# Optimization experiments

Hardware: AMD Instinct MI355X
Metric: run time of the kernel (lower is better)

The kernel has to match this reference:

```python
import jax, jax.numpy as jnp
import numpy as np

B, CIN, H, W = 8, 3, 128, 128
D_MODEL = 256
N_LAYERS = 4
D_STATE = 16
D_CONV = 4
EXPAND = 2
HEADDIM = 64
D_INNER = EXPAND * D_MODEL            # 512
NHEADS = D_INNER // HEADDIM           # 8
CONV_DIM = D_INNER + 2 * D_STATE      # 544
D_IN_PROJ = 2 * D_INNER + 2 * D_STATE + NHEADS  # 1064
D_OUT = 10
EPS = 1e-5


def setup_inputs() -> dict:
    key = jax.random.key(0)
    ks = iter(jax.random.split(key, 64))
    nrm = lambda shape, s=0.02: jax.random.normal(next(ks), shape, jnp.float32) * s
    L = N_LAYERS
    # dt init in [1e-3, 0.1], dt_bias = inverse softplus of dt
    dt = jnp.exp(jax.random.uniform(next(ks), (L, NHEADS)) * (np.log(0.1) - np.log(1e-3)) + np.log(1e-3))
    dt_bias = dt + jnp.log(-jnp.expm1(-dt))
    A_log = jnp.log(jax.random.uniform(next(ks), (L, NHEADS), minval=1.0, maxval=16.0))
    return {
        "x": jax.random.normal(next(ks), (B, CIN, H, W), jnp.float32),
        "stem_w1": nrm((D_MODEL // 2, CIN, 3, 3), 0.1),
        "stem_g1": jnp.ones((D_MODEL // 2,), jnp.float32),
        "stem_b1": jnp.zeros((D_MODEL // 2,), jnp.float32),
        "stem_w2": nrm((D_MODEL, D_MODEL // 2, 4, 4), 0.05),
        "stem_g2": jnp.ones((D_MODEL,), jnp.float32),
        "stem_b2": jnp.zeros((D_MODEL,), jnp.float32),
        "in_w": nrm((L, D_MODEL, D_IN_PROJ)),
        "conv_w": nrm((L, CONV_DIM, D_CONV), 0.2),
        "conv_b": jnp.zeros((L, CONV_DIM), jnp.float32),
        "dt_bias": dt_bias,
        "A_log": A_log,
        "D_skip": jnp.ones((L, NHEADS), jnp.float32),
        "rms_w": jnp.ones((L, D_INNER), jnp.float32),
        "out_w": nrm((L, D_INNER, D_MODEL)),
        "ln_g": jnp.ones((L, D_MODEL), jnp.float32),
        "ln_b": jnp.zeros((L, D_MODEL), jnp.float32),
        "head_ln_g": jnp.ones((D_MODEL,), jnp.float32),
        "head_ln_b": jnp.zeros((D_MODEL,), jnp.float32),
        "head_w": nrm((D_MODEL, D_OUT)),
        "head_b": jnp.zeros((D_OUT,), jnp.float32),
    }


def _bn(x, g, b):  # eval-mode BatchNorm2d with running mean 0 / var 1
    return x * g[None, :, None, None] + b[None, :, None, None]


def _ln(x, g, b):
    m = jnp.mean(x, -1, keepdims=True)
    v = jnp.mean((x - m) ** 2, -1, keepdims=True)
    return (x - m) * jax.lax.rsqrt(v + EPS) * g + b


def _mamba2(x, in_w, conv_w, conv_b, dt_bias, A_log, D_skip, rms_w, out_w):
    Bb, Lq, _ = x.shape
    zxbcdt = x @ in_w                                        # (B,L,D_IN_PROJ)
    z = zxbcdt[..., :D_INNER]
    xBC = zxbcdt[..., D_INNER:D_INNER + CONV_DIM]
    dt = jax.nn.softplus(zxbcdt[..., -NHEADS:] + dt_bias)    # (B,L,H)
    # causal depthwise conv1d over time
    xp = jnp.pad(xBC, ((0, 0), (D_CONV - 1, 0), (0, 0)))
    xBC = sum(xp[:, k:k + Lq, :] * conv_w[:, k] for k in range(D_CONV)) + conv_b
    xBC = jax.nn.silu(xBC)
    xs = xBC[..., :D_INNER].reshape(Bb, Lq, NHEADS, HEADDIM)       # (B,L,H,P)
    Bm = xBC[..., D_INNER:D_INNER + D_STATE]                        # (B,L,N)
    Cm = xBC[..., D_INNER + D_STATE:]                               # (B,L,N)
    dA = jnp.exp(dt * (-jnp.exp(A_log)))                            # (B,L,H)
    dtx = xs * dt[..., None]                                        # (B,L,H,P)

    def step(h, inp):  # h: (B,H,P,N)
        dA_t, dtx_t, B_t, C_t = inp
        h = h * dA_t[:, :, None, None] + dtx_t[..., None] * B_t[:, None, None, :]
        y = jnp.einsum('bhpn,bn->bhp', h, C_t)
        return h, y

    h0 = jnp.zeros((Bb, NHEADS, HEADDIM, D_STATE), x.dtype)
    seq = (jnp.moveaxis(dA, 1, 0), jnp.moveaxis(dtx, 1, 0),
           jnp.moveaxis(Bm, 1, 0), jnp.moveaxis(Cm, 1, 0))
    _, ys = jax.lax.scan(step, h0, seq)                             # (L,B,H,P)
    y = jnp.moveaxis(ys, 0, 1) + xs * D_skip[None, None, :, None]
    y = y.reshape(Bb, Lq, D_INNER)
    y = y * jax.nn.silu(z)                                          # gated
    y = y * jax.lax.rsqrt(jnp.mean(y * y, -1, keepdims=True) + EPS) * rms_w
    return y @ out_w


def reference(x, stem_w1, stem_g1, stem_b1, stem_w2, stem_g2, stem_b2,
              in_w, conv_w, conv_b, dt_bias, A_log, D_skip, rms_w, out_w,
              ln_g, ln_b, head_ln_g, head_ln_b, head_w, head_b):
    dn = ('NCHW', 'OIHW', 'NCHW')
    h = jax.lax.conv_general_dilated(x, stem_w1, (1, 1), 'SAME', dimension_numbers=dn)
    h = jax.nn.gelu(_bn(h, stem_g1, stem_b1), approximate=False)
    h = jax.lax.conv_general_dilated(h, stem_w2, (4, 4), 'VALID', dimension_numbers=dn)
    h = jax.nn.gelu(_bn(h, stem_g2, stem_b2), approximate=False)
    tok = h.reshape(h.shape[0], D_MODEL, -1).transpose(0, 2, 1)     # (B,L,D)
    for i in range(N_LAYERS):
        m = _mamba2(tok, in_w[i], conv_w[i], conv_b[i], dt_bias[i],
                    A_log[i], D_skip[i], rms_w[i], out_w[i])
        tok = _ln(m + tok, ln_g[i], ln_b[i])
    pooled = tok.mean(1)
    return _ln(pooled, head_ln_g, head_ln_b) @ head_w + head_b
```

## Files before the change

kernel.cpp:

```cpp
#include <hip/hip_runtime.h>
#include <hip/hip_bf16.h>


#define DEV __device__ __forceinline__
typedef __hip_bfloat16 bf16;
typedef unsigned short ushort_t;
typedef __attribute__((ext_vector_type(8))) short s8v;
typedef __attribute__((ext_vector_type(8))) unsigned short u8v;
typedef __attribute__((ext_vector_type(4))) unsigned short u4v;
typedef __attribute__((ext_vector_type(4))) float f4v;

#define CHUNK 32
#define NCH 32

#define SP_CONVW 0
#define SP_CONVB 8704
#define SP_DTB   10880
#define SP_ALOG  10912
#define SP_DSK   10944
#define SP_RMSW  10976
#define SP_LNG   13024
#define SP_LNB   14048
#define SP_HLG   15072
#define SP_HLB   15328
#define SP_HW    15584
#define SP_HB    18144
#define SP_G1    18160
#define SP_B1    18288
#define SP_G2    18416
#define SP_B2    18672
#define SP_TOTAL 18928

DEV float bf2f(bf16 h) { return __bfloat162float(h); }
DEV bf16 f2bf(float f) { return __float2bfloat16(f); }
DEV float us2f(ushort_t u) { return __uint_as_float(((unsigned int)u) << 16); }
DEV ushort_t f2bfs(float f) {
    unsigned int u = __float_as_uint(f);
    return (ushort_t)((u + 0x7FFFu + ((u >> 16) & 1u)) >> 16);
}
DEV float ldf(const void* p, size_t i, int bf) {
    return bf ? us2f(((const ushort_t*)p)[i]) : ((const float*)p)[i];
}
DEV ushort_t ldbf(const void* p, size_t i, int bf) {
    return bf ? ((const ushort_t*)p)[i] : f2bfs(((const float*)p)[i]);
}
DEV int mode_of(const void* g1) { return (((const unsigned int*)g1)[0] == 0x3F800000u) ? 0 : 1; }
DEV float sigmoidf_(float x) { return 1.f / (1.f + __expf(-x)); }
DEV float geluf_(float x) { return 0.5f * x * (1.f + erff(x * 0.70710678118654752f)); }

__global__ void k_prep(const void* cw, const void* cb, const void* dtb, const void* alog,
                       const void* dsk, const void* rmsw, const void* lng, const void* lnb,
                       const void* hlg, const void* hlb, const void* hw, const void* hb,
                       const void* g1, const void* b1, const void* g2, const void* b2,
                       const void* w1, const void* w2, const void* inw, const void* outw,
                       float* __restrict__ sp, ushort_t* __restrict__ wT) {
    int md = mode_of(g1);
    int i = blockIdx.x * 256 + threadIdx.x;
    if (i < SP_TOTAL) {
        float v;
        if (i < SP_CONVB) v = ldf(cw, i, md);
        else if (i < SP_DTB) v = ldf(cb, i - SP_CONVB, md);
        else if (i < SP_ALOG) v = ldf(dtb, i - SP_DTB, md);
        else if (i < SP_DSK) v = ldf(alog, i - SP_ALOG, md);
        else if (i < SP_RMSW) v = ldf(dsk, i - SP_DSK, md);
        else if (i < SP_LNG) v = ldf(rmsw, i - SP_RMSW, md);
        else if (i < SP_LNB) v = ldf(lng, i - SP_LNG, md);
        else if (i < SP_HLG) v = ldf(lnb, i - SP_LNB, md);
        else if (i < SP_HLB) v = ldf(hlg, i - SP_HLG, md);
        else if (i < SP_HW) v = ldf(hlb, i - SP_HLB, md);
        else if (i < SP_HB) v = ldf(hw, i - SP_HW, md);
        else if (i < SP_G1) v = (i - SP_HB < 10) ? ldf(hb, i - SP_HB, md) : 0.f;
        else if (i < SP_B1) v = ldf(g1, i - SP_G1, md);
        else if (i < SP_G2) v = ldf(b1, i - SP_B1, md);
        else if (i < SP_B2) v = ldf(g2, i - SP_G2, md);
        else v = ldf(b2, i - SP_B2, md);
        sp[i] = v;
        return;
    }
    int iw = i - SP_TOTAL;
    if (iw >= 2142208) return;
    ushort_t v;
    if (iw < 4096) {
        int oc = iw >> 5, k = iw & 31;
        v = (k < 27) ? ldbf(w1, (size_t)oc * 27 + k, md) : 0;
    } else if (iw < 528384) {
        int j = iw - 4096;
        int oc = j >> 11, k = j & 2047;
        int c = k & 127, kykx = k >> 7;
        v = ldbf(w2, (size_t)(oc * 128 + c) * 16 + kykx, md);
    } else if (iw < 1617920) {
        int j = iw - 528384;
        int l = j / 272384, r = j % 272384;
        int n = r >> 8, k = r & 255;
        v = ldbf(inw, (size_t)l * 272384 + (size_t)k * 1064 + n, md);
    } else {
        int j = iw - 1617920;
        int l = j >> 17, r = j & 131071;
        int n = r >> 9, k = r & 511;
        v = ldbf(outw, (size_t)l * 131072 + (size_t)k * 256 + n, md);
    }
    wT[iw] = v;
}

template <int MD>
DEV void im2col_body(const void* x, ushort_t* __restrict__ Aim, int m) {
    int xx = m & 127;
    int y = (m >> 7) & 127;
    int b = m >> 14;
    ushort_t* o = Aim + (size_t)m * 32;
#pragma unroll
    for (int ci = 0; ci < 3; ci++)
#pragma unroll
        for (int dy = 0; dy < 3; dy++) {
            int sy = y + dy - 1;
#pragma unroll
            for (int dx = 0; dx < 3; dx++) {
                int sx = xx + dx - 1;
                ushort_t v = 0;
                if (sy >= 0 && sy < 128 && sx >= 0 && sx < 128) {
                    size_t idx = (size_t)((b * 3 + ci) * 128 + sy) * 128 + sx;
                    v = MD ? ((const ushort_t*)x)[idx] : f2bfs(((const float*)x)[idx]);
                }
                o[ci * 9 + dy * 3 + dx] = v;
            }
        }
#pragma unroll
    for (int k = 27; k < 32; k++) o[k] = 0;
}
__global__ void k_im2col(const void* __restrict__ x, ushort_t* __restrict__ Aim,
                         const void* __restrict__ g1) {
    int m = blockIdx.x * 256 + threadIdx.x;
    if (m >= 131072) return;
    if (mode_of(g1)) im2col_body<1>(x, Aim, m);
    else im2col_body<0>(x, Aim, m);
}

template <int EPI, int CBF, int BK>
__global__ __launch_bounds__(256, 3) void k_gemmT(const ushort_t* __restrict__ A,
                                                  const ushort_t* __restrict__ Wt, void* __restrict__ C,
                                                  int M, int N, int K, int klen,
                                                  const float* __restrict__ g, const float* __restrict__ bb) {
    constexpr int KG = BK / 8;
    constexpr int EA = BK / 4;
    constexpr int EB = BK / 2;
    constexpr int AU = EA / 8;
    constexpr int BU = EB / 8;
    __shared__ __align__(16) ushort_t As[2][64 * BK];
    __shared__ __align__(16) ushort_t Bs[2][128 * BK];
    int tid = threadIdx.x;
    int m0 = blockIdx.y * 64, n0 = blockIdx.x * 128;
    int koff = blockIdx.z * klen;
    int w = tid >> 6, lane = tid & 63;
    int wm = (w >> 1) * 32, wn = (w & 1) * 64;
    int lm = lane & 15, quad = lane >> 4;
    int ar = tid >> 2, ak = (tid & 3) * EA;
    int br = tid >> 1, bk = (tid & 1) * EB;
    bool bvalid = (n0 + br) < N;

    u8v pa[AU], pb[BU];
    auto loadT = [&](int kb) {
        const u8v* ap = (const u8v*)(A + (size_t)(m0 + ar) * K + koff + kb + ak);
#pragma unroll
        for (int j = 0; j < AU; j++) pa[j] = ap[j];
        if (bvalid) {
            const u8v* bp = (const u8v*)(Wt + (size_t)(n0 + br) * K + koff + kb + bk);
#pragma unroll
            for (int j = 0; j < BU; j++) pb[j] = bp[j];
        } else {
#pragma unroll
            for (int j = 0; j < BU; j++) pb[j] = (u8v)0;
        }
    };
    auto storeT = [&](int buf) {
        int ag = ak >> 3;
#pragma unroll
        for (int j = 0; j < AU; j++)
            *(u8v*)&As[buf][((ar >> 4) * KG + ag + j) * 128 + (ar & 15) * 8] = pa[j];
        int bg = bk >> 3;
#pragma unroll
        for (int j = 0; j < BU; j++)
            *(u8v*)&Bs[buf][((br >> 4) * KG + bg + j) * 128 + (br & 15) * 8] = pb[j];
    };

    f4v acc[2][4];
#pragma unroll
    for (int i = 0; i < 2; i++)
#pragma unroll
        for (int j = 0; j < 4; j++) acc[i][j] = (f4v){0.f, 0.f, 0.f, 0.f};

    int niter = klen / BK;
    loadT(0);
    storeT(0);
    if (niter > 1) loadT(BK);
    __syncthreads();
    for (int it = 0; it < niter; it++) {
        int buf = it & 1;
        if (it + 1 < niter) {
            storeT(buf ^ 1);
            if (it + 2 < niter) loadT((it + 2) * BK);
        }
#pragma unroll
        for (int kk = 0; kk < BK / 32; kk++) {
            s8v af[2], bfr[4];
#pragma unroll
            for (int i = 0; i < 2; i++)
                af[i] = *(const s8v*)&As[buf][(((wm >> 4) + i) * KG + kk * 4 + quad) * 128 + lm * 8];
#pragma unroll
            for (int j = 0; j < 4; j++)
                bfr[j] = *(const s8v*)&Bs[buf][(((wn >> 4) + j) * KG + kk * 4 + quad) * 128 + lm * 8];
#pragma unroll
            for (int i = 0; i < 2; i++)
#pragma unroll
                for (int j = 0; j < 4; j++)
                    acc[i][j] = __builtin_amdgcn_mfma_f32_16x16x32_bf16(af[i], bfr[j], acc[i][j], 0, 0, 0);
        }
        __syncthreads();
    }
    float* Cz = (float*)C + (size_t)blockIdx.z * M * N;
#pragma unroll
    for (int i = 0; i < 2; i++)
#pragma unroll
        for (int j = 0; j < 4; j++) {
            int nn = n0 + wn + j * 16 + lm;
            if (nn >= N) continue;
            float gv = (EPI >= 1) ? g[nn] : 0.f, bv = (EPI >= 1) ? bb[nn] : 0.f;
#pragma unroll
            for (int rr = 0; rr < 4; rr++) {
                int mm = m0 + wm + i * 16 + quad * 4 + rr;
                float v = acc[i][j][rr];
                if (EPI >= 1) v = geluf_(v * gv + bv);
                if (EPI == 2) {
                    int b = mm >> 14, y = (mm >> 7) & 127, x = mm & 127;
                    size_t mp = (size_t)(b * 1024 + (y >> 2) * 32 + (x >> 2));
                    ((bf16*)C)[mp * 2048 + ((y & 3) * 4 + (x & 3)) * 128 + nn] = f2bf(v);
                } else if (CBF) {
                    ((bf16*)C)[(size_t)mm * N + nn] = f2bf(v);
                } else {
                    Cz[(size_t)mm * N + nn] = v;
                }
            }
        }
}

__global__ __launch_bounds__(256) void k_stemred(const float* __restrict__ parts, const float* __restrict__ sp,
                                                 float* __restrict__ tok, ushort_t* __restrict__ tokb) {
    int m = blockIdx.x, c = threadIdx.x;
    size_t off = (size_t)m * 256 + c;
    float s = parts[off] + parts[2097152 + off];
    float v = geluf_(s * sp[SP_G2 + c] + sp[SP_B2 + c]);
    tok[off] = v;
    tokb[off] = f2bfs(v);
}

__global__ __launch_bounds__(64) void k_scan1(const bf16* __restrict__ zx, const float* __restrict__ sp,
                                              float* __restrict__ Sbuf, float* __restrict__ Pbuf, int layer) {
    int bid = blockIdx.x;
    int c = bid & (NCH - 1);
    int bh = bid >> 5;
    int b = bh >> 3, h = bh & 7;
    int p = threadIdx.x;
    __shared__ __align__(16) ushort_t zraw[35 * 64];
    __shared__ __align__(16) ushort_t braw[35 * 32];
    __shared__ float xs_s[CHUNK * 64];
    __shared__ __align__(16) float bc_s[CHUNK * 32];
    __shared__ float da_s[CHUNK], dt_s[CHUNK];
    const ushort_t* zxB = (const ushort_t*)zx + (size_t)b * 1024 * 1064;
    int t0 = c * CHUNK;
#pragma unroll
    for (int k = 0; k < 5; k++) {
        int j = p + k * 64;
        if (j < 280) {
            int row = j >> 3, c8 = j & 7;
            int t = t0 - 3 + row;
            u8v v = (u8v)0;
            if (t >= 0) v = *(const u8v*)(zxB + (size_t)t * 1064 + 512 + h * 64 + c8 * 8);
            *(u8v*)&zraw[row * 64 + c8 * 8] = v;
        }
    }
#pragma unroll
    for (int k = 0; k < 3; k++) {
        int j = p + k * 64;
        if (j < 140) {
            int row = j >> 2, c8 = j & 3;
            int t = t0 - 3 + row;
            u8v v = (u8v)0;
            if (t >= 0) v = *(const u8v*)(zxB + (size_t)t * 1064 + 1024 + c8 * 8);
            *(u8v*)&braw[row * 32 + c8 * 8] = v;
        }
    }
    if (p < CHUNK) {
        float raw = bf2f(zx[(size_t)(b * 1024 + t0 + p) * 1064 + 1056 + h]) + sp[SP_DTB + layer * 8 + h];
        float dt = raw > 20.f ? raw : log1pf(expf(raw));
        float a = expf(sp[SP_ALOG + layer * 8 + h]);
        dt_s[p] = dt;
        da_s[p] = expf(-dt * a);
    }
    __syncthreads();
    {
        const float* wp = sp + SP_CONVW + (size_t)(layer * 544 + h * 64 + p) * 4;
        float w0 = wp[0], w1 = wp[1], w2 = wp[2], w3 = wp[3];
        float bias = sp[SP_CONVB + layer * 544 + h * 64 + p];
#pragma unroll 8
        for (int tt = 0; tt < CHUNK; tt++) {
            float acc = bias + us2f(zraw[tt * 64 + p]) * w0 + us2f(zraw[(tt + 1) * 64 + p]) * w1 +
                        us2f(zraw[(tt + 2) * 64 + p]) * w2 + us2f(zraw[(tt + 3) * 64 + p]) * w3;
            xs_s[tt * 64 + p] = acc * sigmoidf_(acc);
        }
    }
    if (p < 32) {
        const float* wp = sp + SP_CONVW + (size_t)(layer * 544 + 512 + p) * 4;
        float w0 = wp[0], w1 = wp[1], w2 = wp[2], w3 = wp[3];
        float bias = sp[SP_CONVB + layer * 544 + 512 + p];
        int n = p & 15;
        int slot = (p < 16) ? 2 * n : 2 * n + 1;
#pragma unroll 8
        for (int tt = 0; tt < CHUNK; tt++) {
            float acc = bias + us2f(braw[tt * 32 + p]) * w0 + us2f(braw[(tt + 1) * 32 + p]) * w1 +
                        us2f(braw[(tt + 2) * 32 + p]) * w2 + us2f(braw[(tt + 3) * 32 + p]) * w3;
            bc_s[tt * 32 + slot] = acc * sigmoidf_(acc);
        }
    }
    __syncthreads();
    float hs[16];
#pragma unroll
    for (int n = 0; n < 16; n++) hs[n] = 0.f;
    float P = 1.f;
    for (int tt = 0; tt < CHUNK; tt++) {
        float xsv = xs_s[tt * 64 + p];
        float dAv = da_s[tt], dtv = dt_s[tt];
        P *= dAv;
        float dtx = xsv * dtv;
        const float4* bcp = (const float4*)&bc_s[tt * 32];
#pragma unroll
        for (int j = 0; j < 8; j++) {
            float4 v = bcp[j];
            hs[2 * j] = hs[2 * j] * dAv + dtx * v.x;
            hs[2 * j + 1] = hs[2 * j + 1] * dAv + dtx * v.z;
        }
    }
    float* So = Sbuf + (size_t)bid * 1024;
#pragma unroll
    for (int n = 0; n < 16; n++) So[n * 64 + p] = hs[n];
    if (p == 0) Pbuf[bid] = P;
}

__global__ __launch_bounds__(256) void k_scan2(const float* __restrict__ Sbuf, const float* __restrict__ Pbuf,
                                               float* __restrict__ Hbuf) {
    int bh = blockIdx.x >> 2;
    int e = ((blockIdx.x & 3) << 8) + threadIdx.x;
    const float* Sp = Sbuf + (size_t)bh * NCH * 1024 + e;
    float* Hp = Hbuf + (size_t)bh * NCH * 1024 + e;
    float hh = 0.f;
#pragma unroll
    for (int gq = 0; gq < 4; gq++) {
        float s[8];
#pragma unroll
        for (int c2 = 0; c2 < 8; c2++) s[c2] = Sp[(size_t)(gq * 8 + c2) * 1024];
#pragma unroll
        for (int c2 = 0; c2 < 8; c2++) {
            Hp[(size_t)(gq * 8 + c2) * 1024] = hh;
            float P = Pbuf[bh * NCH + gq * 8 + c2];
            hh = P * hh + s[c2];
        }
    }
}

__global__ __launch_bounds__(512, 2) void k_scan3g(const bf16* __restrict__ zx,
                                                   const float* __restrict__ Hbuf,
                                                   const float* __restrict__ sp, bf16* __restrict__ y,
                                                   int layer) {
    int bid = blockIdx.x;
    int c = bid & 31;
    int b = bid >> 5;
    int tid = threadIdx.x;
    int h = tid >> 6, p = tid & 63;
    __shared__ __align__(16) ushort_t zraw[35 * 512];
    __shared__ __align__(16) ushort_t braw[35 * 32];
    __shared__ __align__(16) float bc_s[CHUNK * 32];
    __shared__ float da_s[8 * CHUNK], dt_s[8 * CHUNK];
    const ushort_t* zxB = (const ushort_t*)zx + (size_t)b * 1024 * 1064;
    int t0 = c * CHUNK;

#pragma unroll
    for (int k = 0; k < 5; k++) {
        int j = tid + k * 512;
        if (j < 2240) {
            int row = j >> 6, c8 = j & 63;
            int t = t0 - 3 + row;
            u8v v = (u8v)0;
            if (t >= 0) v = *(const u8v*)(zxB + (size_t)t * 1064 + 512 + c8 * 8);
            *(u8v*)&zraw[row * 512 + c8 * 8] = v;
        }
    }
    if (tid < 140) {
        int row = tid >> 2, c8 = tid & 3;
        int t = t0 - 3 + row;
        u8v v = (u8v)0;
        if (t >= 0) v = *(const u8v*)(zxB + (size_t)t * 1064 + 1024 + c8 * 8);
        *(u8v*)&braw[row * 32 + c8 * 8] = v;
    }
    if (tid < 256) {
        int tt = tid >> 3, hh = tid & 7;
        float raw = bf2f(zx[(size_t)(b * 1024 + t0 + tt) * 1064 + 1056 + hh]) + sp[SP_DTB + layer * 8 + hh];
        float dtv = raw > 20.f ? raw : log1pf(expf(raw));
        float a = expf(sp[SP_ALOG + layer * 8 + hh]);
        dt_s[hh * 32 + tt] = dtv;
        da_s[hh * 32 + tt] = expf(-dtv * a);
    }
    __syncthreads();

    float xs[CHUNK];
    {
        float4 w4 = *(const float4*)(sp + SP_CONVW + (size_t)(layer * 544 + tid) * 4);
        float bias = sp[SP_CONVB + layer * 544 + tid];
#pragma unroll
        for (int tt = 0; tt < CHUNK; tt++) {
            float acc = bias + us2f(zraw[tt * 512 + tid]) * w4.x + us2f(zraw[(tt + 1) * 512 + tid]) * w4.y +
                        us2f(zraw[(tt + 2) * 512 + tid]) * w4.z + us2f(zraw[(tt + 3) * 512 + tid]) * w4.w;
            xs[tt] = acc * sigmoidf_(acc);
        }
    }
    if (tid < 32) {
        float4 w4 = *(const float4*)(sp + SP_CONVW + (size_t)(layer * 544 + 512 + tid) * 4);
        float bias = sp[SP_CONVB + layer * 544 + 512 + tid];
        int n = tid & 15;
        int slot = (tid < 16) ? 2 * n : 2 * n + 1;
#pragma unroll
        for (int tt = 0; tt < CHUNK; tt++) {
            float acc = bias + us2f(braw[tt * 32 + tid]) * w4.x + us2f(braw[(tt + 1) * 32 + tid]) * w4.y +
                        us2f(braw[(tt + 2) * 32 + tid]) * w4.z + us2f(braw[(tt + 3) * 32 + tid]) * w4.w;
            bc_s[tt * 32 + slot] = acc * sigmoidf_(acc);
        }
    }

    float hs[16];
    {
        const float* Si = Hbuf + ((size_t)(b * 8 + h) * 32 + c) * 1024;
#pragma unroll
        for (int n = 0; n < 16; n++) hs[n] = Si[n * 64 + p];
    }
    float dsk = sp[SP_DSK + layer * 8 + h];
    __syncthreads();

    ushort_t* y_s = zraw;
#pragma unroll
    for (int tt = 0; tt < CHUNK; tt++) {
        float dAv = da_s[h * 32 + tt], dtv = dt_s[h * 32 + tt];
        float dtx = xs[tt] * dtv;
        float acc = 0.f;
        const float4* bcp = (const float4*)&bc_s[tt * 32];
#pragma unroll
        for (int j = 0; j < 8; j++) {
            float4 v = bcp[j];
            hs[2 * j] = hs[2 * j] * dAv + dtx * v.x;
            acc += hs[2 * j] * v.y;
            hs[2 * j + 1] = hs[2 * j + 1] * dAv + dtx * v.z;
            acc += hs[2 * j + 1] * v.w;
        }
        y_s[tt * 512 + tid] = f2bfs(acc + xs[tt] * dsk);
    }
    __syncthreads();

    {
        int lane = p;
        float4 rw0 = *(const float4*)(sp + SP_RMSW + layer * 512 + lane * 8);
        float4 rw1 = *(const float4*)(sp + SP_RMSW + layer * 512 + lane * 8 + 4);
        float rwv[8] = {rw0.x, rw0.y, rw0.z, rw0.w, rw1.x, rw1.y, rw1.z, rw1.w};
#pragma unroll
        for (int r = 0; r < 4; r++) {
            int tt = h * 4 + r;
            u8v yv = *(const u8v*)&y_s[tt * 512 + lane * 8];
            u8v zv = *(const u8v*)(zxB + (size_t)(t0 + tt) * 1064 + lane * 8);
            float t[8];
            float ss = 0.f;
#pragma unroll
            for (int j2 = 0; j2 < 8; j2++) {
                float z = us2f(zv[j2]);
                float yy = us2f(yv[j2]);
                float tv = yy * (z * sigmoidf_(z));
                t[j2] = tv;
                ss += tv * tv;
            }
#pragma unroll
            for (int d = 32; d; d >>= 1) ss += __shfl_xor(ss, d, 64);
            float scale = rsqrtf(ss * (1.f / 512.f) + 1e-5f);
            u8v o;
#pragma unroll
            for (int j2 = 0; j2 < 8; j2++) o[j2] = f2bfs(t[j2] * scale * rwv[j2]);
            *(u8v*)((ushort_t*)y + (size_t)(b * 1024 + t0 + tt) * 512 + lane * 8) = o;
        }
    }
}

DEV float block_sum256(float v, float* s4) {
#pragma unroll
    for (int off = 32; off; off >>= 1) v += __shfl_down(v, off, 64);
    __syncthreads();
    if ((threadIdx.x & 63) == 0) s4[threadIdx.x >> 6] = v;
    __syncthreads();
    return s4[0] + s4[1] + s4[2] + s4[3];
}

__global__ __launch_bounds__(256) void k_resln(float* __restrict__ tok, ushort_t* __restrict__ tokb,
                                               const float* __restrict__ parts, const float* __restrict__ sp,
                                               int layer) {
    int w = threadIdx.x >> 6, lane = threadIdx.x & 63;
    int m = blockIdx.x * 4 + w;
    size_t off = (size_t)m * 256 + lane * 4;
    float4 v = *(const float4*)(tok + off);
    float4 p0 = *(const float4*)(parts + off);
    float4 p1 = *(const float4*)(parts + 2097152 + off);
    v.x += p0.x + p1.x;
    v.y += p0.y + p1.y;
    v.z += p0.z + p1.z;
    v.w += p0.w + p1.w;
    float s = v.x + v.y + v.z + v.w;
#pragma unroll
    for (int d = 32; d; d >>= 1) s += __shfl_xor(s, d, 64);
    float mean = s * (1.f / 256.f);
    float dx = v.x - mean, dy = v.y - mean, dz = v.z - mean, dw = v.w - mean;
    float ss = dx * dx + dy * dy + dz * dz + dw * dw;
#pragma unroll
    for (int d = 32; d; d >>= 1) ss += __shfl_xor(ss, d, 64);
    float inv = rsqrtf(ss * (1.f / 256.f) + 1e-5f);
    const float* lg = sp + SP_LNG + layer * 256 + lane * 4;
    const float* lb = sp + SP_LNB + layer * 256 + lane * 4;
    float r0 = dx * inv * lg[0] + lb[0];
    float r1 = dy * inv * lg[1] + lb[1];
    float r2 = dz * inv * lg[2] + lb[2];
    float r3 = dw * inv * lg[3] + lb[3];
    float4 r;
    r.x = r0; r.y = r1; r.z = r2; r.w = r3;
    *(float4*)(tok + off) = r;
    u4v ob;
    ob[0] = f2bfs(r0); ob[1] = f2bfs(r1); ob[2] = f2bfs(r2); ob[3] = f2bfs(r3);
    *(u4v*)(tokb + off) = ob;
}

__global__ void k_pool1(const float* __restrict__ tok, float* __restrict__ ppart) {
    int b = blockIdx.x >> 4, chunk = blockIdx.x & 15;
    int c = threadIdx.x;
    float s = 0.f;
    for (int t = 0; t < 64; t++) s += tok[((size_t)b * 1024 + chunk * 64 + t) * 256 + c];
    ppart[(size_t)blockIdx.x * 256 + c] = s;
}

__global__ __launch_bounds__(256) void k_head(const float* __restrict__ ppart, const float* __restrict__ sp,
                                              void* __restrict__ out, const void* __restrict__ g1) {
    __shared__ float s4[4];
    __shared__ float lds[256];
    int md = mode_of(g1);
    int b = blockIdx.x;
    int c = threadIdx.x;
    float v = 0.f;
#pragma unroll
    for (int k = 0; k < 16; k++) v += ppart[(size_t)(b * 16 + k) * 256 + c];
    v *= (1.f / 1024.f);
    float mean = block_sum256(v, s4) * (1.f / 256.f);
    float d = v - mean;
    float var = block_sum256(d * d, s4) * (1.f / 256.f);
    lds[c] = d * rsqrtf(var + 1e-5f) * sp[SP_HLG + c] + sp[SP_HLB + c];
    __syncthreads();
    if (c < 10) {
        float s = sp[SP_HB + c];
        for (int k = 0; k < 256; k++) s += lds[k] * sp[SP_HW + k * 10 + c];
        if (md)
            ((bf16*)out)[b * 10 + c] = f2bf(s);
        else
            ((float*)out)[b * 10 + c] = s;
    }
}

extern "C" void kernel_launch(void* const* d_in, const int* in_sizes, int n_in, void* d_out, int out_size,
                              void* d_ws, size_t ws_size, hipStream_t stream) {
    const void* x         = d_in[0];
    const void* stem_w1   = d_in[1];
    const void* stem_g1   = d_in[2];
    const void* stem_b1   = d_in[3];
    const void* stem_w2   = d_in[4];
    const void* stem_g2   = d_in[5];
    const void* stem_b2   = d_in[6];
    const void* in_w      = d_in[7];
    const void* conv_w    = d_in[8];
    const void* conv_b    = d_in[9];
    const void* dt_bias   = d_in[10];
    const void* A_log     = d_in[11];
    const void* D_skip    = d_in[12];
    const void* rms_w     = d_in[13];
    const void* out_w     = d_in[14];
    const void* ln_g      = d_in[15];
    const void* ln_b      = d_in[16];
    const void* head_ln_g = d_in[17];
    const void* head_ln_b = d_in[18];
    const void* head_w    = d_in[19];
    const void* head_b    = d_in[20];

    float* ws     = (float*)d_ws;
    float* tok    = ws;
    float* mbuf   = ws + 2097152;
    float* Hbuf   = ws + 4194304;
    float* parts  = ws + 6291456;
    float* ppart  = ws + 14682112;
    float* Pbuf   = ws + 14714880;
    float* sp     = ws + 14716944;
    ushort_t* tokb = (ushort_t*)(ws + 14735888);
    ushort_t* wT  = (ushort_t*)(ws + 15784464);
    ushort_t* w1T   = wT;
    ushort_t* w2T   = wT + 4096;
    ushort_t* inwT  = wT + 528384;
    ushort_t* outwT = wT + 1617920;
    bf16* arena   = (bf16*)(ws + 16855568);
    bf16* zx      = arena;
    bf16* ybuf    = arena + 13172736;
    ushort_t* patch = (ushort_t*)arena;
    ushort_t* Aim  = (ushort_t*)mbuf;
    float* Sbuf    = mbuf;

    k_prep<<<(SP_TOTAL + 2142208 + 255) / 256, 256, 0, stream>>>(
        conv_w, conv_b, dt_bias, A_log, D_skip, rms_w, ln_g, ln_b, head_ln_g, head_ln_b, head_w, head_b,
        stem_g1, stem_b1, stem_g2, stem_b2, stem_w1, stem_w2, in_w, out_w, sp, wT);

    k_im2col<<<512, 256, 0, stream>>>(x, Aim, stem_g1);
    k_gemmT<2, 1, 32><<<dim3(1, 2048, 1), 256, 0, stream>>>(Aim, w1T, patch, 131072, 128, 32, 32,
                                                            sp + SP_G1, sp + SP_B1);
    k_gemmT<0, 0, 64><<<dim3(2, 128, 2), 256, 0, stream>>>(patch, w2T, parts, 8192, 256, 2048, 1024,
                                                           nullptr, nullptr);
    k_stemred<<<8192, 256, 0, stream>>>(parts, sp, tok, tokb);

    for (int l = 0; l < 4; l++) {
        k_gemmT<0, 1, 64><<<dim3(9, 128, 1), 256, 0, stream>>>(tokb, inwT + (size_t)l * 272384, zx, 8192,
                                                               1064, 256, 256, nullptr, nullptr);
        k_scan1<<<2048, 64, 0, stream>>>(zx, sp, Sbuf, Pbuf, l);
        k_scan2<<<256, 256, 0, stream>>>(Sbuf, Pbuf, Hbuf);
        k_scan3g<<<256, 512, 0, stream>>>(zx, Hbuf, sp, ybuf, l);
        k_gemmT<0, 0, 64><<<dim3(2, 128, 2), 256, 0, stream>>>((const ushort_t*)ybuf,
                                                               outwT + (size_t)l * 131072, parts, 8192, 256,
                                                               512, 256, nullptr, nullptr);
        k_resln<<<8192 / 4, 256, 0, stream>>>(tok, tokb, parts, sp, l);
    }

    k_pool1<<<128, 256, 0, stream>>>(tok, ppart);
    k_head<<<8, 256, 0, stream>>>(ppart, sp, d_out, stem_g1);
}
```

Measured before the change: 483.1 us.

## Add 128x128 double-buffered MFMA GEMM for stem and in-projection

Adds a new GEMM kernel with 128x128 output tiles, register-prefetched double-buffered shared memory, and each wave computing a 64x64 sub-tile with bf16 MFMA. The stem second conv and the per-layer in-projection use it, and the stem conv split-K goes from 2 to 4 partial slices, so the reduction kernel now sums four partial buffers. The aim is more reuse per loaded tile and fewer global loads. The cost is higher register and LDS use per block, a larger parts buffer, and extra reduction traffic. The out-projection GEMM is left on the old kernel.

```diff
diff --git a/kernel.cpp b/kernel.cpp
--- a/kernel.cpp
+++ b/kernel.cpp
@@ -242,11 +242,102 @@
         }
 }
 
+template <int CBF>
+__global__ __launch_bounds__(256, 2) void k_gemm128(const ushort_t* __restrict__ A,
+                                                    const ushort_t* __restrict__ Wt, void* __restrict__ C,
+                                                    int M, int N, int K, int klen) {
+    constexpr int BK = 64;
+    constexpr int KG = BK / 8;
+    __shared__ __align__(16) ushort_t As[2][128 * BK];
+    __shared__ __align__(16) ushort_t Bs[2][128 * BK];
+    int tid = threadIdx.x;
+    int m0 = blockIdx.y * 128, n0 = blockIdx.x * 128;
+    int koff = blockIdx.z * klen;
+    int w = tid >> 6, lane = tid & 63;
+    int wm = (w >> 1) * 64, wn = (w & 1) * 64;
+    int lm = lane & 15, quad = lane >> 4;
+    int r = tid >> 1, ck = (tid & 1) * 32;
+    bool bvalid = (n0 + r) < N;
+
+    u8v pa[4], pb[4];
+    auto loadT = [&](int kb) {
+        const u8v* ap = (const u8v*)(A + (size_t)(m0 + r) * K + koff + kb + ck);
+#pragma unroll
+        for (int j = 0; j < 4; j++) pa[j] = ap[j];
+        if (bvalid) {
+            const u8v* bp = (const u8v*)(Wt + (size_t)(n0 + r) * K + koff + kb + ck);
+#pragma unroll
+            for (int j = 0; j < 4; j++) pb[j] = bp[j];
+        } else {
+#pragma unroll
+            for (int j = 0; j < 4; j++) pb[j] = (u8v)0;
+        }
+    };
+    auto storeT = [&](int buf) {
+        int g = ck >> 3;
+#pragma unroll
+        for (int j = 0; j < 4; j++) {
+            *(u8v*)&As[buf][((r >> 4) * KG + g + j) * 128 + (r & 15) * 8] = pa[j];
+            *(u8v*)&Bs[buf][((r >> 4) * KG + g + j) * 128 + (r & 15) * 8] = pb[j];
+        }
+    };
+
+    f4v acc[4][4];
+#pragma unroll
+    for (int i = 0; i < 4; i++)
+#pragma unroll
+        for (int j = 0; j < 4; j++) acc[i][j] = (f4v){0.f, 0.f, 0.f, 0.f};
+
+    int niter = klen / BK;
+    loadT(0);
+    storeT(0);
+    if (niter > 1) loadT(BK);
+    __syncthreads();
+    for (int it = 0; it < niter; it++) {
+        int buf = it & 1;
+        if (it + 1 < niter) {
+            storeT(buf ^ 1);
+            if (it + 2 < niter) loadT((it + 2) * BK);
+        }
+#pragma unroll
+        for (int kk = 0; kk < 2; kk++) {
+            s8v af[4], bfr[4];
+#pragma unroll
+            for (int i = 0; i < 4; i++)
+                af[i] = *(const s8v*)&As[buf][(((wm >> 4) + i) * KG + kk * 4 + quad) * 128 + lm * 8];
+#pragma unroll
+            for (int j = 0; j < 4; j++)
+                bfr[j] = *(const s8v*)&Bs[buf][(((wn >> 4) + j) * KG + kk * 4 + quad) * 128 + lm * 8];
+#pragma unroll
+            for (int i = 0; i < 4; i++)
+#pragma unroll
+                for (int j = 0; j < 4; j++)
+                    acc[i][j] = __builtin_amdgcn_mfma_f32_16x16x32_bf16(af[i], bfr[j], acc[i][j], 0, 0, 0);
+        }
+        __syncthreads();
+    }
+    float* Cz = (float*)C + (size_t)blockIdx.z * M * N;
+#pragma unroll
+    for (int i = 0; i < 4; i++)
+#pragma unroll
+        for (int j = 0; j < 4; j++) {
+            int nn = n0 + wn + j * 16 + lm;
+            if (nn >= N) continue;
+#pragma unroll
+            for (int rr = 0; rr < 4; rr++) {
+                int mm = m0 + wm + i * 16 + quad * 4 + rr;
+                float v = acc[i][j][rr];
+                if (CBF) ((bf16*)C)[(size_t)mm * N + nn] = f2bf(v);
+                else Cz[(size_t)mm * N + nn] = v;
+            }
+        }
+}
+
 __global__ __launch_bounds__(256) void k_stemred(const float* __restrict__ parts, const float* __restrict__ sp,
                                                  float* __restrict__ tok, ushort_t* __restrict__ tokb) {
     int m = blockIdx.x, c = threadIdx.x;
     size_t off = (size_t)m * 256 + c;
-    float s = parts[off] + parts[2097152 + off];
+    float s = parts[off] + parts[2097152 + off] + parts[2 * 2097152 + off] + parts[3 * 2097152 + off];
     float v = geluf_(s * sp[SP_G2 + c] + sp[SP_B2 + c]);
     tok[off] = v;
     tokb[off] = f2bfs(v);
@@ -623,13 +714,12 @@
     k_im2col<<<512, 256, 0, stream>>>(x, Aim, stem_g1);
     k_gemmT<2, 1, 32><<<dim3(1, 2048, 1), 256, 0, stream>>>(Aim, w1T, patch, 131072, 128, 32, 32,
                                                             sp + SP_G1, sp + SP_B1);
-    k_gemmT<0, 0, 64><<<dim3(2, 128, 2), 256, 0, stream>>>(patch, w2T, parts, 8192, 256, 2048, 1024,
-                                                           nullptr, nullptr);
+    k_gemm128<0><<<dim3(2, 64, 4), 256, 0, stream>>>(patch, w2T, parts, 8192, 256, 2048, 512);
     k_stemred<<<8192, 256, 0, stream>>>(parts, sp, tok, tokb);
 
     for (int l = 0; l < 4; l++) {
-        k_gemmT<0, 1, 64><<<dim3(9, 128, 1), 256, 0, stream>>>(tokb, inwT + (size_t)l * 272384, zx, 8192,
-                                                               1064, 256, 256, nullptr, nullptr);
+        k_gemm128<1><<<dim3(9, 64, 1), 256, 0, stream>>>(tokb, inwT + (size_t)l * 272384, zx, 8192,
+                                                         1064, 256, 256);
         k_scan1<<<2048, 64, 0, stream>>>(zx, sp, Sbuf, Pbuf, l);
         k_scan2<<<256, 256, 0, stream>>>(Sbuf, Pbuf, Hbuf);
         k_scan3g<<<256, 512, 0, stream>>>(zx, Hbuf, sp, ybuf, l);
```

Result: no change. 491.6 us (+1.8%).

## Fuse out-projection GEMM and residual LayerNorm into the scan-output kernel

Applied to the files above, without the earlier changes.

The scan-output kernel now keeps its gated, RMS-normalised y chunk (32 tokens × 512) in padded LDS. It runs the out-projection there with bf16 MFMA, each of the 8 waves computing 32 output columns against weights read from global memory. It then adds the residual and applies LayerNorm in place, which removes the y buffer round trip, the split-K partial sums and two kernel launches per layer. The cost is that each block re-reads the full 256KB out-projection weight from global/L2 with only 256 blocks, and the LDS row stride is padded to avoid bank conflicts.

```diff
diff --git a/kernel.cpp b/kernel.cpp
--- a/kernel.cpp
+++ b/kernel.cpp
@@ -12,6 +12,7 @@
 
 #define CHUNK 32
 #define NCH 32
+#define YST 520
 
 #define SP_CONVW 0
 #define SP_CONVB 8704
@@ -365,10 +366,12 @@
     }
 }
 
-__global__ __launch_bounds__(512, 2) void k_scan3g(const bf16* __restrict__ zx,
-                                                   const float* __restrict__ Hbuf,
-                                                   const float* __restrict__ sp, bf16* __restrict__ y,
-                                                   int layer) {
+__global__ __launch_bounds__(512, 2) void k_scan3go(const bf16* __restrict__ zx,
+                                                    const float* __restrict__ Hbuf,
+                                                    const float* __restrict__ sp,
+                                                    const ushort_t* __restrict__ Wt,
+                                                    float* __restrict__ tok, ushort_t* __restrict__ tokb,
+                                                    int layer) {
     int bid = blockIdx.x;
     int c = bid & 31;
     int b = bid >> 5;
@@ -457,7 +460,7 @@
             hs[2 * j + 1] = hs[2 * j + 1] * dAv + dtx * v.z;
             acc += hs[2 * j + 1] * v.w;
         }
-        y_s[tt * 512 + tid] = f2bfs(acc + xs[tt] * dsk);
+        y_s[tt * YST + tid] = f2bfs(acc + xs[tt] * dsk);
     }
     __syncthreads();
 
@@ -469,7 +472,7 @@
 #pragma unroll
         for (int r = 0; r < 4; r++) {
             int tt = h * 4 + r;
-            u8v yv = *(const u8v*)&y_s[tt * 512 + lane * 8];
+            u8v yv = *(const u8v*)&y_s[tt * YST + lane * 8];
             u8v zv = *(const u8v*)(zxB + (size_t)(t0 + tt) * 1064 + lane * 8);
             float t[8];
             float ss = 0.f;
@@ -487,8 +490,75 @@
             u8v o;
 #pragma unroll
             for (int j2 = 0; j2 < 8; j2++) o[j2] = f2bfs(t[j2] * scale * rwv[j2]);
-            *(u8v*)((ushort_t*)y + (size_t)(b * 1024 + t0 + tt) * 512 + lane * 8) = o;
-        }
+            *(u8v*)&y_s[tt * YST + lane * 8] = o;
+        }
+    }
+    __syncthreads();
+
+    int lm = p & 15, quad = p >> 4;
+    f4v acc2[2][2];
+#pragma unroll
+    for (int mi = 0; mi < 2; mi++)
+#pragma unroll
+        for (int ni = 0; ni < 2; ni++) acc2[mi][ni] = (f4v){0.f, 0.f, 0.f, 0.f};
+#pragma unroll
+    for (int kk = 0; kk < 16; kk++) {
+        s8v af[2], bw[2];
+#pragma unroll
+        for (int mi = 0; mi < 2; mi++)
+            af[mi] = *(const s8v*)&y_s[(mi * 16 + lm) * YST + kk * 32 + quad * 8];
+#pragma unroll
+        for (int ni = 0; ni < 2; ni++)
+            bw[ni] = *(const s8v*)(Wt + (size_t)(h * 32 + ni * 16 + lm) * 512 + kk * 32 + quad * 8);
+#pragma unroll
+        for (int mi = 0; mi < 2; mi++)
+#pragma unroll
+            for (int ni = 0; ni < 2; ni++)
+                acc2[mi][ni] = __builtin_amdgcn_mfma_f32_16x16x32_bf16(af[mi], bw[ni], acc2[mi][ni], 0, 0, 0);
+    }
+    __syncthreads();
+
+    float* C_lds = (float*)zraw;
+#pragma unroll
+    for (int mi = 0; mi < 2; mi++)
+#pragma unroll
+        for (int ni = 0; ni < 2; ni++)
+#pragma unroll
+            for (int rr = 0; rr < 4; rr++)
+                C_lds[(mi * 16 + quad * 4 + rr) * 260 + h * 32 + ni * 16 + lm] = acc2[mi][ni][rr];
+    __syncthreads();
+
+#pragma unroll
+    for (int r = 0; r < 4; r++) {
+        int tt = h * 4 + r;
+        size_t off = (size_t)(b * 1024 + t0 + tt) * 256 + p * 4;
+        float4 v = *(const float4*)(tok + off);
+        float4 cv = *(const float4*)&C_lds[tt * 260 + p * 4];
+        v.x += cv.x;
+        v.y += cv.y;
+        v.z += cv.z;
+        v.w += cv.w;
+        float s = v.x + v.y + v.z + v.w;
+#pragma unroll
+        for (int d = 32; d; d >>= 1) s += __shfl_xor(s, d, 64);
+        float mean = s * (1.f / 256.f);
+        float dx = v.x - mean, dy = v.y - mean, dz = v.z - mean, dw = v.w - mean;
+        float ss = dx * dx + dy * dy + dz * dz + dw * dw;
+#pragma unroll
+        for (int d = 32; d; d >>= 1) ss += __shfl_xor(ss, d, 64);
+        float inv = rsqrtf(ss * (1.f / 256.f) + 1e-5f);
+        const float* lg = sp + SP_LNG + layer * 256 + p * 4;
+        const float* lb = sp + SP_LNB + layer * 256 + p * 4;
+        float r0 = dx * inv * lg[0] + lb[0];
+        float r1 = dy * inv * lg[1] + lb[1];
+        float r2 = dz * inv * lg[2] + lb[2];
+        float r3 = dw * inv * lg[3] + lb[3];
+        float4 rv;
+        rv.x = r0; rv.y = r1; rv.z = r2; rv.w = r3;
+        *(float4*)(tok + off) = rv;
+        u4v ob;
+        ob[0] = f2bfs(r0); ob[1] = f2bfs(r1); ob[2] = f2bfs(r2); ob[3] = f2bfs(r3);
+        *(u4v*)(tokb + off) = ob;
     }
 }
 
@@ -499,42 +569,6 @@
     if ((threadIdx.x & 63) == 0) s4[threadIdx.x >> 6] = v;
     __syncthreads();
     return s4[0] + s4[1] + s4[2] + s4[3];
-}
-
-__global__ __launch_bounds__(256) void k_resln(float* __restrict__ tok, ushort_t* __restrict__ tokb,
-                                               const float* __restrict__ parts, const float* __restrict__ sp,
-                                               int layer) {
-    int w = threadIdx.x >> 6, lane = threadIdx.x & 63;
-    int m = blockIdx.x * 4 + w;
-    size_t off = (size_t)m * 256 + lane * 4;
-    float4 v = *(const float4*)(tok + off);
-    float4 p0 = *(const float4*)(parts + off);
-    float4 p1 = *(const float4*)(parts + 2097152 + off);
-    v.x += p0.x + p1.x;
-    v.y += p0.y + p1.y;
-    v.z += p0.z + p1.z;
-    v.w += p0.w + p1.w;
-    float s = v.x + v.y + v.z + v.w;
-#pragma unroll
-    for (int d = 32; d; d >>= 1) s += __shfl_xor(s, d, 64);
-    float mean = s * (1.f / 256.f);
-    float dx = v.x - mean, dy = v.y - mean, dz = v.z - mean, dw = v.w - mean;
-    float ss = dx * dx + dy * dy + dz * dz + dw * dw;
-#pragma unroll
-    for (int d = 32; d; d >>= 1) ss += __shfl_xor(ss, d, 64);
-    float inv = rsqrtf(ss * (1.f / 256.f) + 1e-5f);
-    const float* lg = sp + SP_LNG + layer * 256 + lane * 4;
-    const float* lb = sp + SP_LNB + layer * 256 + lane * 4;
-    float r0 = dx * inv * lg[0] + lb[0];
-    float r1 = dy * inv * lg[1] + lb[1];
-    float r2 = dz * inv * lg[2] + lb[2];
-    float r3 = dw * inv * lg[3] + lb[3];
-    float4 r;
-    r.x = r0; r.y = r1; r.z = r2; r.w = r3;
-    *(float4*)(tok + off) = r;
-    u4v ob;
-    ob[0] = f2bfs(r0); ob[1] = f2bfs(r1); ob[2] = f2bfs(r2); ob[3] = f2bfs(r3);
-    *(u4v*)(tokb + off) = ob;
 }
 
 __global__ void k_pool1(const float* __restrict__ tok, float* __restrict__ ppart) {
@@ -611,7 +645,6 @@
     ushort_t* outwT = wT + 1617920;
     bf16* arena   = (bf16*)(ws + 16855568);
     bf16* zx      = arena;
-    bf16* ybuf    = arena + 13172736;
     ushort_t* patch = (ushort_t*)arena;
     ushort_t* Aim  = (ushort_t*)mbuf;
     float* Sbuf    = mbuf;
@@ -632,11 +665,7 @@
                                                                1064, 256, 256, nullptr, nullptr);
         k_scan1<<<2048, 64, 0, stream>>>(zx, sp, Sbuf, Pbuf, l);
         k_scan2<<<256, 256, 0, stream>>>(Sbuf, Pbuf, Hbuf);
-        k_scan3g<<<256, 512, 0, stream>>>(zx, Hbuf, sp, ybuf, l);
-        k_gemmT<0, 0, 64><<<dim3(2, 128, 2), 256, 0, stream>>>((const ushort_t*)ybuf,
-                                                               outwT + (size_t)l * 131072, parts, 8192, 256,
-                                                               512, 256, nullptr, nullptr);
-        k_resln<<<8192 / 4, 256, 0, stream>>>(tok, tokb, parts, sp, l);
+        k_scan3go<<<256, 512, 0, stream>>>(zx, Hbuf, sp, outwT + (size_t)l * 131072, tok, tokb, l);
     }
 
     k_pool1<<<128, 256, 0, stream>>>(tok, ppart);
```

After: 461.8 us. 4.4% less time.
